# Performance work log

Hardware: AMD Instinct MI355X
Metric: run time of the kernel (lower is better)

The kernel has to match this reference:

```python
import jax, jax.numpy as jnp
import numpy as np
from jax import lax

FI, FO, K, EPS = 512, 256, 3, 1e-06


def _fir_kernel(gain):
    f = jnp.array([1.0, 3.0, 3.0, 1.0], dtype=jnp.float32)
    f = f[None, :] * f[:, None]
    f = f / f.sum() * gain  # (4,4), symmetric so conv-vs-correlation flip is a no-op
    return f


def setup_inputs() -> dict:
    key = jax.random.key(0)
    k1, k2 = jax.random.split(key)
    x = jax.random.normal(k1, (8, FI, 64, 64), dtype=jnp.float32)
    w = jax.random.normal(k2, (1, FO, FI, K, K), dtype=jnp.float32)
    return {"x": x, "w": w}


def reference(x, w):
    w_scale = (FI * K * K) ** (-0.5)
    wm = w[0] * w_scale  # (fo, fi, k, k); per-sample scale is constant across batch
    demod = lax.rsqrt(jnp.sum(wm * wm, axis=(1, 2, 3)) + EPS)  # (fo,)
    wm = wm * demod[:, None, None, None]
    # torch conv_transpose2d(stride=2, padding=0) with weight (fi, fo, k, k) where
    # weight[i, o] = wm[o, i]  ==  dilated conv with kernel flip(wm) OIHW, pad k-1=2.
    kern = wm[:, :, ::-1, ::-1]
    y = lax.conv_general_dilated(
        x, kern, window_strides=(1, 1), padding=[(2, 2), (2, 2)],
        lhs_dilation=(2, 2), dimension_numbers=("NCHW", "OIHW", "NCHW"))
    # upFirDn2D with scale=2, conv_k=3: p=0 -> pad (1,1) both dims, filter gain 4
    f = _fir_kernel(4.0)
    C = y.shape[1]
    fk = jnp.broadcast_to(f[None, None], (C, 1, 4, 4))
    y = lax.conv_general_dilated(
        y, fk, window_strides=(1, 1), padding=[(1, 1), (1, 1)],
        feature_group_count=C, dimension_numbers=("NCHW", "OIHW", "NCHW"))
    return y  # (8, 256, 128, 128)
```

## Files before the change

kernel.cpp:

```cpp
#include <hip/hip_runtime.h>

typedef unsigned short u16;
typedef unsigned int u32;
typedef __attribute__((ext_vector_type(8))) short bf16x8;
typedef __attribute__((ext_vector_type(4))) float f32x4;

#define XP_BYTES 35684352
#define YB_BYTES 68714544
#define HY_OFF   (XP_BYTES + YB_BYTES)
#define WS_NEED  ((size_t)HY_OFF + 2359296)
#define CS 16776

__device__ inline u16 f2bf(float f) {
  union { float f; unsigned u; } v; v.f = f;
  unsigned r = v.u + 0x7fffu + ((v.u >> 16) & 1u);
  return (u16)(r >> 16);
}

__device__ inline void gl_lds16(const u16* g, u16* l) {
  __builtin_amdgcn_global_load_lds(
      (const __attribute__((address_space(1))) unsigned int*)g,
      (__attribute__((address_space(3))) unsigned int*)l, 16, 0, 0);
}

__global__ void xprep(const float* __restrict__ x, u16* __restrict__ xp) {
  __shared__ float tile[64 * 65];
  int bid = blockIdx.x;
  int cc = bid & 7, h = (bid >> 3) & 63, n = bid >> 9;
  int c0 = cc * 64;
  int t = threadIdx.x;
  const float* xb = x + ((size_t)(n * 512 + c0) * 64 + h) * 64;
  for (int r = 0; r < 16; ++r) {
    int flat = r * 256 + t;
    int ci = flat >> 6, w = flat & 63;
    tile[w * 65 + ci] = xb[(size_t)ci * 4096 + w];
  }
  __syncthreads();
  u16* xpb = xp + ((size_t)(n * 66 + h + 1) * 66 + 1) * 512 + c0;
  for (int r = 0; r < 8; ++r) {
    int flat = r * 256 + t;
    int pr = flat & 31;
    int w = flat >> 5;
    int ci = pr * 2;
    float v0 = tile[w * 65 + ci], v1 = tile[w * 65 + ci + 1];
    unsigned pk = (unsigned)f2bf(v0) | ((unsigned)f2bf(v1) << 16);
    *(unsigned*)(xpb + (size_t)w * 512 + ci) = pk;
  }
  u16* rowbase = xp + ((size_t)(n * 66 + h + 1) * 66) * 512 + c0;
  if (t < 32) *(u32*)(rowbase + 2 * t) = 0u;
  else if (t < 64) *(u32*)(rowbase + (size_t)65 * 512 + 2 * (t - 32)) = 0u;
  if (h == 0) {
    u16* r0 = xp + ((size_t)(n * 66) * 66) * 512 + c0;
    for (int j = t; j < 2112; j += 256) {
      int col = j >> 5, wi = j & 31;
      *(u32*)(r0 + (size_t)col * 512 + 2 * wi) = 0u;
    }
  }
  if (h == 63) {
    u16* r65 = xp + ((size_t)(n * 66 + 65) * 66) * 512 + c0;
    for (int j = t; j < 2112; j += 256) {
      int col = j >> 5, wi = j & 31;
      *(u32*)(r65 + (size_t)col * 512 + 2 * wi) = 0u;
    }
  }
}

__global__ void wprep9(const float* __restrict__ w, u16* __restrict__ Hy) {
  __shared__ float wl[4608];
  __shared__ float red[256];
  int o = blockIdx.x, t = threadIdx.x;
  const float* wo = w + (size_t)o * 4608;
  float s = 0.f;
  for (int j = t; j < 4608; j += 256) { float v = wo[j]; wl[j] = v; s += v * v; }
  red[t] = s;
  __syncthreads();
  for (int st = 128; st; st >>= 1) { if (t < st) red[t] += red[t + st]; __syncthreads(); }
  float demod = rsqrtf(red[0] * (1.0f / 4608.0f) + 1e-6f);
  float scale = demod * 0.014731391274719739f;
  const int DY[9] = {0, 2, 0, 2, 0, 2, 1, 1, 1};
  const int DX[9] = {0, 0, 2, 2, 1, 1, 0, 2, 1};
  for (int i = t; i < 512; i += 256) {
#pragma unroll
    for (int pl = 0; pl < 9; ++pl) {
      float g = wl[i * 9 + DY[pl] * 3 + DX[pl]] * scale;
      Hy[(size_t)pl * 131072 + (size_t)o * 512 + i] = f2bf(g);
    }
  }
}

#define BARR() __builtin_amdgcn_s_barrier()
#define WAITL() do { asm volatile("s_waitcnt lgkmcnt(0)" ::: "memory"); __builtin_amdgcn_sched_barrier(0); } while (0)
#define WAITV1() do { asm volatile("s_waitcnt vmcnt(1)" ::: "memory"); __builtin_amdgcn_sched_barrier(0); } while (0)
#define WAITV0() do { asm volatile("s_waitcnt vmcnt(0)" ::: "memory"); __builtin_amdgcn_sched_barrier(0); } while (0)

__device__ __forceinline__ void rdA4(const u16* sbA, int la, int grp, int hi,
                                     bf16x8 af[4]) {
#pragma unroll
  for (int ti = 0; ti < 4; ++ti) {
    int p = ti * 16 + la;
    int slot = (hi * 4 + grp) ^ (p & 7);
    af[ti] = *(const bf16x8*)(sbA + p * 64 + slot * 8);
  }
}

__device__ __forceinline__ bf16x8 rdB1(const u16* sb, int r, int grp) {
  int p = r & 63, hi = r >> 6;
  int slot = (hi * 4 + grp) ^ (p & 7);
  return *(const bf16x8*)(sb + 8192 + p * 64 + slot * 8);
}

template <int MI, int NI>
__device__ __forceinline__ void qmfma4(const bf16x8 af[4], bf16x8 bf,
                                       f32x4 acc[8][2]) {
#pragma unroll
  for (int ti = 0; ti < 4; ++ti)
    acc[MI * 4 + ti][NI] = __builtin_amdgcn_mfma_f32_16x16x32_bf16(
        af[ti], bf, acc[MI * 4 + ti][NI], 0, 0, 0);
}

__device__ __forceinline__ void stA1(const u16* __restrict__ xp, u16* d,
                                     int tile, int NK, u32 a,
                                     u32 adj1, u32 adj2, u32 adj3) {
  if (tile < NK) {
    int tap = tile >> 4;
    u32 ko = (u32)((tile & 15) << 5);
    u32 adj = tap == 0 ? 0u : (tap == 1 ? adj1 : (tap == 2 ? adj2 : adj3));
    gl_lds16(xp + (a - adj + ko), d);
  }
}

__device__ __forceinline__ void stB1(const u16* __restrict__ hb, u16* d,
                                     int tile, int NK, u32 b) {
  if (tile < NK) {
    int tap = tile >> 4;
    u32 ko = (u32)((tile & 15) << 5);
    gl_lds16(hb + (size_t)tap * 131072 + (b + ko), d);
  }
}

__global__ __launch_bounds__(512, 4) void conv_y(const u16* __restrict__ xp,
                                                 const u16* __restrict__ Hy,
                                                 u16* __restrict__ yb) {
  __shared__ __align__(16) u16 su[24576];

  int bid = blockIdx.x;
  int t = threadIdx.x;
  int wid = t >> 6, lane = t & 63;

  int img = bid & 7;
  int kk = bid >> 3;
  int mt, oh, Wp, CNT, NTAP, PB, PO, STLIM;
  u32 adj1 = 0, adj2 = 0, adj3 = 0;
  if (kk < 34)       { int k2 = kk;       mt = k2 >> 1; oh = k2 & 1; Wp = 66; CNT = 4290; NTAP = 4; PB = 0; PO = 0;     STLIM = 4296;
                       adj1 = 33792u; adj2 = 512u; adj3 = 34304u; }
  else if (kk < 68)  { int k2 = kk - 34;  mt = k2 >> 1; oh = k2 & 1; Wp = 64; CNT = 4160; NTAP = 2; PB = 4; PO = 4296;  STLIM = 4160;
                       adj1 = 33792u; }
  else if (kk < 102) { int k2 = kk - 68;  mt = k2 >> 1; oh = k2 & 1; Wp = 66; CNT = 4224; NTAP = 2; PB = 6; PO = 8456;  STLIM = 4224;
                       adj1 = 512u; }
  else               { int k2 = kk - 102; mt = k2 >> 1; oh = k2 & 1; Wp = 64; CNT = 4096; NTAP = 1; PB = 8; PO = 12680; STLIM = 4096; }

  int m0 = mt * 256;
  int o0 = oh * 128;
  int NK = NTAP * 16;
  int NITER = NTAP * 8;
  const u16* hb = Hy + (size_t)PB * 131072;

  int wm = wid >> 2, wn = wid & 3;
  int la = lane & 15, grp = lane >> 4;

  int sp = t >> 3;
  int se = (t & 7) ^ (sp & 7);
  int shi = se >> 2, sc = se & 3;
  int sloc = shi * 64 + sp;

  u32 gA0, gA1, gB;
  {
    int m = m0 + sloc;
    if (m > CNT - 1) m = CNT - 1;
    u32 a = (u32)m / (u32)Wp;
    u32 b = (u32)m - a * (u32)Wp;
    gA0 = (u32)(((img * 66 + a + 1) * 66 + (b + 1)) * 512 + sc * 8);
    m = m0 + 128 + sloc;
    if (m > CNT - 1) m = CNT - 1;
    a = (u32)m / (u32)Wp;
    b = (u32)m - a * (u32)Wp;
    gA1 = (u32)(((img * 66 + a + 1) * 66 + (b + 1)) * 512 + sc * 8);
    gB = (u32)((o0 + sloc) * 512 + sc * 8);
  }
  int ws = wid * 512;

  f32x4 acc[8][2];
#pragma unroll
  for (int i = 0; i < 8; ++i)
#pragma unroll
    for (int j = 0; j < 2; ++j) acc[i][j] = (f32x4){0.f, 0.f, 0.f, 0.f};

  stB1(hb, su + 8192 + ws, 0, NK, gB);
  stA1(xp, su + 0 + ws, 0, NK, gA0, adj1, adj2, adj3);
  stA1(xp, su + 4096 + ws, 0, NK, gA1, adj1, adj2, adj3);
  stB1(hb, su + 20480 + ws, 1, NK, gB);
  WAITV1();
  BARR();

  bf16x8 af[4], bf0, bf1;

#pragma unroll 1
  for (int it = 0; it < NITER; ++it) {
    int t0 = 2 * it;
    bool more = (it + 1 < NITER);

    rdA4(su + wm * 4096, la, grp, 0, af);
    bf0 = rdB1(su, wn * 32 + la, grp);
    stA1(xp, su + 12288 + ws, t0 + 1, NK, gA0, adj1, adj2, adj3);
    BARR(); WAITL();
    __builtin_amdgcn_s_setprio(1); qmfma4<0, 0>(af, bf0, acc); __builtin_amdgcn_s_setprio(0);
    BARR();
    bf1 = rdB1(su, wn * 32 + 16 + la, grp);
    stA1(xp, su + 16384 + ws, t0 + 1, NK, gA1, adj1, adj2, adj3);
    BARR(); WAITL();
    __builtin_amdgcn_s_setprio(1); qmfma4<0, 1>(af, bf1, acc); __builtin_amdgcn_s_setprio(0);
    BARR();
    rdA4(su + wm * 4096, la, grp, 1, af);
    stB1(hb, su + 8192 + ws, t0 + 2, NK, gB);
    BARR(); WAITL();
    __builtin_amdgcn_s_setprio(1);
    qmfma4<1, 1>(af, bf1, acc); qmfma4<1, 0>(af, bf0, acc);
    __builtin_amdgcn_s_setprio(0);
    if (more) { WAITV1(); } else { WAITV0(); }
    BARR();
    rdA4(su + 12288 + wm * 4096, la, grp, 0, af);
    bf0 = rdB1(su + 12288, wn * 32 + la, grp);
    stA1(xp, su + 0 + ws, t0 + 2, NK, gA0, adj1, adj2, adj3);
    BARR(); WAITL();
    __builtin_amdgcn_s_setprio(1); qmfma4<0, 0>(af, bf0, acc); __builtin_amdgcn_s_setprio(0);
    BARR();
    bf1 = rdB1(su + 12288, wn * 32 + 16 + la, grp);
    stA1(xp, su + 4096 + ws, t0 + 2, NK, gA1, adj1, adj2, adj3);
    BARR(); WAITL();
    __builtin_amdgcn_s_setprio(1); qmfma4<0, 1>(af, bf1, acc); __builtin_amdgcn_s_setprio(0);
    BARR();
    rdA4(su + 12288 + wm * 4096, la, grp, 1, af);
    stB1(hb, su + 20480 + ws, t0 + 3, NK, gB);
    BARR(); WAITL();
    __builtin_amdgcn_s_setprio(1);
    qmfma4<1, 1>(af, bf1, acc); qmfma4<1, 0>(af, bf0, acc);
    __builtin_amdgcn_s_setprio(0);
    if (more) { WAITV1(); }
    BARR();
  }

  WAITV0();
  __syncthreads();
  u16* ybp = yb + 8;
#pragma unroll 1
  for (int r = 0; r < 2; ++r) {
    if ((wn >> 1) == r) {
      int base_orl = (wn & 1) * 32;
#pragma unroll
      for (int nj = 0; nj < 2; ++nj) {
        int orl = base_orl + nj * 16 + la;
        int x7 = orl & 7;
#pragma unroll
        for (int mi8 = 0; mi8 < 8; ++mi8)
#pragma unroll
          for (int jp = 0; jp < 2; ++jp) {
            int ml = wm * 128 + mi8 * 16 + grp * 4 + jp * 2;
            u32 pk = (u32)f2bf(acc[mi8][nj][jp * 2]) |
                     ((u32)f2bf(acc[mi8][nj][jp * 2 + 1]) << 16);
            *(u32*)(su + orl * 256 + (((ml >> 3) ^ x7) * 8) + (ml & 7)) = pk;
          }
      }
    }
    __syncthreads();
    {
      int ol = t >> 3, s2 = t & 7;
      int og = o0 + r * 64 + ol;
      size_t gb = (size_t)(img * 256 + og) * CS + PO + m0;
      int x7 = ol & 7;
#pragma unroll
      for (int i = 0; i < 4; ++i) {
        int cidx = s2 * 4 + i;
        int m = cidx * 8;
        if (m0 + m < STLIM)
          *(bf16x8*)(ybp + gb + m) = *(const bf16x8*)(su + ol * 256 + ((cidx ^ x7) * 8));
      }
    }
    if (r == 0) __syncthreads();
  }
}

__global__ void fir2(const u16* __restrict__ yb, float* __restrict__ z) {
  int flat = blockIdx.x * 256 + threadIdx.x;
  int qh = flat & 15, phb = (flat >> 4) & 31, o = (flat >> 9) & 255, n = flat >> 17;
  const u16* cb = yb + 8 + (size_t)(n * 256 + o) * CS;
  int a0 = 2 * phb - 1;
  int b0 = 4 * qh - 1;

  float out[4][8];
#pragma unroll
  for (int i = 0; i < 4; ++i)
#pragma unroll
    for (int j = 0; j < 8; ++j) out[i][j] = 0.f;

  const int PO_[4] = {0, 4296, 8456, 12680};
  const int WP_[4] = {66, 64, 66, 64};
  const int HA_[4] = {65, 65, 64, 64};
  const int WB_[4] = {65, 64, 65, 64};

#pragma unroll
  for (int ph = 0; ph < 4; ++ph) {
    int rp = ph >> 1, rq = ph & 1;
    const u16* pb = cb + PO_[ph];
    float hcol[4][8];
#pragma unroll
    for (int la = 0; la < 4; ++la) {
      if (rp == 0 && la == 0) continue;
      int ag = a0 + la;
      bool rv = (ag >= 0) && (ag < HA_[ph]);
      const u16* rb = pb + (ag * WP_[ph] + b0 - 1);
      u32 ls[4];
      ls[0] = *(const u32*)(rb);
      ls[1] = *(const u32*)(rb + 2);
      ls[2] = *(const u32*)(rb + 4);
      ls[3] = *(const u32*)(rb + 6);
      float v[6];
#pragma unroll
      for (int lb = 0; lb < 6; ++lb) {
        int jj = lb + 1;
        u32 w16 = (jj & 1) ? (ls[jj >> 1] >> 16) : (ls[jj >> 1] & 0xffffu);
        float fv = __uint_as_float(w16 << 16);
        int bg = b0 + lb;
        bool ok = rv && (bg >= 0) && (bg < WB_[ph]);
        v[lb] = ok ? fv : 0.f;
      }
#pragma unroll
      for (int e = 0; e < 4; ++e) {
        if (rq == 0) {
          hcol[la][2 * e]     = 3.f * v[e + 1] + v[e + 2];
          hcol[la][2 * e + 1] = v[e + 1] + 3.f * v[e + 2];
        } else {
          hcol[la][2 * e]     = v[e] + 3.f * v[e + 1];
          hcol[la][2 * e + 1] = 3.f * v[e + 1] + v[e + 2];
        }
      }
    }
#pragma unroll
    for (int jq = 0; jq < 8; ++jq) {
      if (rp == 0) {
        out[0][jq] += 3.f * hcol[1][jq] + hcol[2][jq];
        out[1][jq] += hcol[1][jq] + 3.f * hcol[2][jq];
        out[2][jq] += 3.f * hcol[2][jq] + hcol[3][jq];
        out[3][jq] += hcol[2][jq] + 3.f * hcol[3][jq];
      } else {
        out[0][jq] += hcol[0][jq] + 3.f * hcol[1][jq];
        out[1][jq] += 3.f * hcol[1][jq] + hcol[2][jq];
        out[2][jq] += hcol[1][jq] + 3.f * hcol[2][jq];
        out[3][jq] += 3.f * hcol[2][jq] + hcol[3][jq];
      }
    }
  }

  float* zb = z + ((size_t)(n * 256 + o) * 128 + phb * 4) * 128 + qh * 8;
#pragma unroll
  for (int ip = 0; ip < 4; ++ip) {
    f32x4 v0, v1;
#pragma unroll
    for (int j = 0; j < 4; ++j) { v0[j] = out[ip][j] * 0.0625f; v1[j] = out[ip][j + 4] * 0.0625f; }
    *(f32x4*)(zb + (size_t)ip * 128) = v0;
    *(f32x4*)(zb + (size_t)ip * 128 + 4) = v1;
  }
}

__global__ void wprep36(const float* __restrict__ w, u16* __restrict__ Hm) {
  __shared__ float wl[4608];
  __shared__ float red[256];
  int o = blockIdx.x, t = threadIdx.x;
  const float* wo = w + (size_t)o * 4608;
  float s = 0.f;
  for (int j = t; j < 4608; j += 256) { float v = wo[j]; wl[j] = v; s += v * v; }
  red[t] = s;
  __syncthreads();
  for (int st = 128; st; st >>= 1) { if (t < st) red[t] += red[t + st]; __syncthreads(); }
  float demod = rsqrtf(red[0] * (1.0f / 4608.0f) + 1e-6f);
  float scale = demod * 0.014731391274719739f;
  const float F1[4] = {1.f, 3.f, 3.f, 1.f};
  for (int i = t; i < 512; i += 256) {
    float wm[9];
    for (int k = 0; k < 9; ++k) wm[k] = wl[i * 9 + k] * scale;
    for (int rp = 0; rp < 2; ++rp)
      for (int rq = 0; rq < 2; ++rq)
        for (int u = 0; u < 3; ++u)
          for (int v = 0; v < 3; ++v) {
            int s_ = 2 - 2 * u + rp, t_ = 2 - 2 * v + rq;
            float g = 0.f;
            for (int dy = 0; dy < 3; ++dy) {
              int a = dy + 1 - s_;
              if (a < 0 || a > 3) continue;
              for (int dx = 0; dx < 3; ++dx) {
                int b = dx + 1 - t_;
                if (b < 0 || b > 3) continue;
                g += wm[dy * 3 + dx] * (F1[a] * F1[b]);
              }
            }
            g *= 0.0625f;
            Hm[(size_t)((rp * 2 + rq) * 9 + u * 3 + v) * 131072 + (size_t)o * 512 + i] = f2bf(g);
          }
  }
}

__global__ __launch_bounds__(256) void conv_main(const u16* __restrict__ xp,
                                                 const u16* __restrict__ Hm,
                                                 float* __restrict__ z) {
  __shared__ __align__(16) float smemf[8448];
  u16* su = (u16*)smemf;
  int bid = blockIdx.x;
  int sub = bid & 7;
  int rp = sub >> 2;
  int o0 = (sub & 3) * 64;
  int mtile = bid >> 3;
  int n_img = mtile >> 5;
  int hp0 = (mtile & 31) * 2;
  int t = threadIdx.x;
  int wave = t >> 6, lane = t & 63;
  int wm0 = (wave & 1) * 64;
  int wn0 = (wave >> 1) * 32;
  int la = lane & 15;
  int ks = (lane >> 4) * 8;
  int rsel = t >> 2;
  int koff = (t & 3) * 8;
  f32x4 acc[2][4][2];
#pragma unroll
  for (int a = 0; a < 2; ++a)
#pragma unroll
    for (int b = 0; b < 4; ++b)
#pragma unroll
      for (int c = 0; c < 2; ++c)
        acc[a][b][c] = (f32x4){0.f, 0.f, 0.f, 0.f};
#pragma unroll 1
  for (int tap = 0; tap < 9; ++tap) {
    int du = tap / 3, dv = tap - du * 3;
    const u16* gA0 = xp + ((size_t)(n_img * 66 + hp0 + du) * 66 + dv) * 512;
    const u16* gB0 = Hm + (size_t)(rp * 18 + tap) * 131072 + (size_t)(o0 + rsel) * 512 + koff;
    const u16* gAr0 = gA0 + (size_t)rsel * 512 + koff;
    const u16* gAr1 = gA0 + (size_t)(66 + rsel) * 512 + koff;
#pragma unroll 1
    for (int kc = 0; kc < 16; ++kc) {
      int c0 = kc * 32;
      __syncthreads();
      gl_lds16(gAr0 + c0, su + wave * 512);
      gl_lds16(gAr1 + c0, su + 2048 + wave * 512);
      gl_lds16(gB0 + c0,              su + 4096 + wave * 512);
      gl_lds16(gB0 + 9 * 131072 + c0, su + 6144 + wave * 512);
      __syncthreads();
      bf16x8 af[4];
#pragma unroll
      for (int ti = 0; ti < 4; ++ti)
        af[ti] = *(const bf16x8*)(su + (wm0 + ti * 16 + la) * 32 + ks);
      bf16x8 bfr[2][2];
#pragma unroll
      for (int rqq = 0; rqq < 2; ++rqq)
#pragma unroll
        for (int tj = 0; tj < 2; ++tj)
          bfr[rqq][tj] = *(const bf16x8*)(su + 4096 + rqq * 2048 + (wn0 + tj * 16 + la) * 32 + ks);
#pragma unroll
      for (int rqq = 0; rqq < 2; ++rqq)
#pragma unroll
        for (int ti = 0; ti < 4; ++ti)
#pragma unroll
          for (int tj = 0; tj < 2; ++tj)
            acc[rqq][ti][tj] = __builtin_amdgcn_mfma_f32_16x16x32_bf16(
                af[ti], bfr[rqq][tj], acc[rqq][ti][tj], 0, 0, 0);
    }
  }
  __syncthreads();
  float* lws = smemf + wave * 2112;
  int p = 2 * (hp0 + (wave & 1)) + rp;
#pragma unroll
  for (int tj = 0; tj < 2; ++tj) {
#pragma unroll
    for (int rqq = 0; rqq < 2; ++rqq)
#pragma unroll
      for (int ti = 0; ti < 4; ++ti) {
        int wqb = ti * 16 + (lane >> 4) * 4;
        f32x4 v = acc[rqq][ti][tj];
#pragma unroll
        for (int r = 0; r < 4; ++r)
          lws[la * 132 + 2 * (wqb + r) + rqq] = v[r];
      }
    __syncthreads();
    int obase = o0 + wn0 + tj * 16;
#pragma unroll
    for (int c = 0; c < 8; ++c) {
      int idx = c * 64 + lane;
      int ol = idx >> 5, q4 = (idx & 31) * 4;
      f32x4 vv = *(const f32x4*)(lws + ol * 132 + q4);
      *(f32x4*)(z + (((size_t)n_img * 256 + obase + ol) * 128 + p) * 128 + q4) = vv;
    }
    __syncthreads();
  }
}

extern "C" void kernel_launch(void* const* d_in, const int* in_sizes, int n_in,
                              void* d_out, int out_size, void* d_ws, size_t ws_size,
                              hipStream_t stream) {
  const float* x = (const float*)d_in[0];
  const float* w = (const float*)d_in[1];
  float* z = (float*)d_out;
  u16* xp = (u16*)d_ws;

  if (ws_size >= WS_NEED) {
    u16* yb = (u16*)((char*)d_ws + XP_BYTES);
    u16* hy = (u16*)((char*)d_ws + HY_OFF);
    xprep<<<4096, 256, 0, stream>>>(x, xp);
    wprep9<<<256, 256, 0, stream>>>(w, hy);
    conv_y<<<1072, 512, 0, stream>>>(xp, hy, yb);
    fir2<<<4096, 256, 0, stream>>>(yb, z);
  } else {
    u16* Hm = (u16*)((char*)d_ws + XP_BYTES);
    hipMemsetAsync(xp, 0, XP_BYTES, stream);
    xprep<<<4096, 256, 0, stream>>>(x, xp);
    wprep36<<<256, 256, 0, stream>>>(w, Hm);
    conv_main<<<2048, 256, 0, stream>>>(xp, Hm, z);
  }
}
```

Before: 322.1 us.

## Switch padded input and weight planes to channel-chunked 32-wide layout

Changes the bf16 padded input from NHWC with 512 contiguous channels to 16 planes of 32-channel chunks per image, and the per-tap weights to matching 32-channel chunk planes. Global-to-LDS loads then fetch from a compact plane per K-tile, which changes how many rows and pages each tile's loads span and may improve cache and TLB locality. The fallback path keeps the old layout through a copied xprep_flat kernel. Stores in xprep become more scattered, and correctness depends on the new offsets matching the LDS tile layout.

```diff
diff --git a/kernel.cpp b/kernel.cpp
--- a/kernel.cpp
+++ b/kernel.cpp
@@ -36,7 +36,6 @@
     tile[w * 65 + ci] = xb[(size_t)ci * 4096 + w];
   }
   __syncthreads();
-  u16* xpb = xp + ((size_t)(n * 66 + h + 1) * 66 + 1) * 512 + c0;
   for (int r = 0; r < 8; ++r) {
     int flat = r * 256 + t;
     int pr = flat & 31;
@@ -44,23 +43,31 @@
     int ci = pr * 2;
     float v0 = tile[w * 65 + ci], v1 = tile[w * 65 + ci + 1];
     unsigned pk = (unsigned)f2bf(v0) | ((unsigned)f2bf(v1) << 16);
-    *(unsigned*)(xpb + (size_t)w * 512 + ci) = pk;
-  }
-  u16* rowbase = xp + ((size_t)(n * 66 + h + 1) * 66) * 512 + c0;
-  if (t < 32) *(u32*)(rowbase + 2 * t) = 0u;
-  else if (t < 64) *(u32*)(rowbase + (size_t)65 * 512 + 2 * (t - 32)) = 0u;
-  if (h == 0) {
-    u16* r0 = xp + ((size_t)(n * 66) * 66) * 512 + c0;
+    int kcabs = cc * 2 + (ci >> 5);
+    int chl = ci & 31;
+    u16* dst = xp + (size_t)(n * 16 + kcabs) * 139392 +
+               (size_t)((h + 1) * 66 + (w + 1)) * 32 + chl;
+    *(unsigned*)dst = pk;
+  }
+  if (t < 64) {
+    int seg = t >> 4;
+    int colsel = (seg >> 1) ? 65 : 0;
+    int pl = cc * 2 + (seg & 1);
+    int ui = t & 15;
+    u16* dst = xp + (size_t)(n * 16 + pl) * 139392 +
+               (size_t)((h + 1) * 66 + colsel) * 32 + ui * 2;
+    *(u32*)dst = 0u;
+  }
+  if (h == 0 || h == 63) {
+    int rowbase = (h == 0) ? 0 : 65 * 66;
     for (int j = t; j < 2112; j += 256) {
-      int col = j >> 5, wi = j & 31;
-      *(u32*)(r0 + (size_t)col * 512 + 2 * wi) = 0u;
-    }
-  }
-  if (h == 63) {
-    u16* r65 = xp + ((size_t)(n * 66 + 65) * 66) * 512 + c0;
-    for (int j = t; j < 2112; j += 256) {
-      int col = j >> 5, wi = j & 31;
-      *(u32*)(r65 + (size_t)col * 512 + 2 * wi) = 0u;
+      int seg = j >> 4;
+      int ui = j & 15;
+      int pl = cc * 2 + (seg & 1);
+      int pos = seg >> 1;
+      u16* dst = xp + (size_t)(n * 16 + pl) * 139392 +
+                 (size_t)(rowbase + pos) * 32 + ui * 2;
+      *(u32*)dst = 0u;
     }
   }
 }
@@ -80,10 +87,11 @@
   const int DY[9] = {0, 2, 0, 2, 0, 2, 1, 1, 1};
   const int DX[9] = {0, 0, 2, 2, 1, 1, 0, 2, 1};
   for (int i = t; i < 512; i += 256) {
+    int kc = i >> 5, il = i & 31;
 #pragma unroll
     for (int pl = 0; pl < 9; ++pl) {
       float g = wl[i * 9 + DY[pl] * 3 + DX[pl]] * scale;
-      Hy[(size_t)pl * 131072 + (size_t)o * 512 + i] = f2bf(g);
+      Hy[(size_t)(pl * 16 + kc) * 8192 + (size_t)o * 32 + il] = f2bf(g);
     }
   }
 }
@@ -123,9 +131,9 @@
                                      u32 adj1, u32 adj2, u32 adj3) {
   if (tile < NK) {
     int tap = tile >> 4;
-    u32 ko = (u32)((tile & 15) << 5);
+    u32 ko = (u32)((tile & 15) * 139392);
     u32 adj = tap == 0 ? 0u : (tap == 1 ? adj1 : (tap == 2 ? adj2 : adj3));
-    gl_lds16(xp + (a - adj + ko), d);
+    gl_lds16(xp + (a + ko - adj), d);
   }
 }
 
@@ -133,8 +141,8 @@
                                      int tile, int NK, u32 b) {
   if (tile < NK) {
     int tap = tile >> 4;
-    u32 ko = (u32)((tile & 15) << 5);
-    gl_lds16(hb + (size_t)tap * 131072 + (b + ko), d);
+    u32 ko = (u32)(tap * 131072 + (tile & 15) * 8192);
+    gl_lds16(hb + (b + ko), d);
   }
 }
 
@@ -152,11 +160,11 @@
   int mt, oh, Wp, CNT, NTAP, PB, PO, STLIM;
   u32 adj1 = 0, adj2 = 0, adj3 = 0;
   if (kk < 34)       { int k2 = kk;       mt = k2 >> 1; oh = k2 & 1; Wp = 66; CNT = 4290; NTAP = 4; PB = 0; PO = 0;     STLIM = 4296;
-                       adj1 = 33792u; adj2 = 512u; adj3 = 34304u; }
+                       adj1 = 2112u; adj2 = 32u; adj3 = 2144u; }
   else if (kk < 68)  { int k2 = kk - 34;  mt = k2 >> 1; oh = k2 & 1; Wp = 64; CNT = 4160; NTAP = 2; PB = 4; PO = 4296;  STLIM = 4160;
-                       adj1 = 33792u; }
+                       adj1 = 2112u; }
   else if (kk < 102) { int k2 = kk - 68;  mt = k2 >> 1; oh = k2 & 1; Wp = 66; CNT = 4224; NTAP = 2; PB = 6; PO = 8456;  STLIM = 4224;
-                       adj1 = 512u; }
+                       adj1 = 32u; }
   else               { int k2 = kk - 102; mt = k2 >> 1; oh = k2 & 1; Wp = 64; CNT = 4096; NTAP = 1; PB = 8; PO = 12680; STLIM = 4096; }
 
   int m0 = mt * 256;
@@ -175,17 +183,18 @@
 
   u32 gA0, gA1, gB;
   {
+    u32 ib = (u32)img * 2230272u;
     int m = m0 + sloc;
     if (m > CNT - 1) m = CNT - 1;
     u32 a = (u32)m / (u32)Wp;
     u32 b = (u32)m - a * (u32)Wp;
-    gA0 = (u32)(((img * 66 + a + 1) * 66 + (b + 1)) * 512 + sc * 8);
+    gA0 = ib + ((a + 1) * 66 + (b + 1)) * 32 + sc * 8;
     m = m0 + 128 + sloc;
     if (m > CNT - 1) m = CNT - 1;
     a = (u32)m / (u32)Wp;
     b = (u32)m - a * (u32)Wp;
-    gA1 = (u32)(((img * 66 + a + 1) * 66 + (b + 1)) * 512 + sc * 8);
-    gB = (u32)((o0 + sloc) * 512 + sc * 8);
+    gA1 = ib + ((a + 1) * 66 + (b + 1)) * 32 + sc * 8;
+    gB = (u32)((o0 + sloc) * 32 + sc * 8);
   }
   int ws = wid * 512;
 
@@ -371,6 +380,48 @@
   }
 }
 
+__global__ void xprep_flat(const float* __restrict__ x, u16* __restrict__ xp) {
+  __shared__ float tile[64 * 65];
+  int bid = blockIdx.x;
+  int cc = bid & 7, h = (bid >> 3) & 63, n = bid >> 9;
+  int c0 = cc * 64;
+  int t = threadIdx.x;
+  const float* xb = x + ((size_t)(n * 512 + c0) * 64 + h) * 64;
+  for (int r = 0; r < 16; ++r) {
+    int flat = r * 256 + t;
+    int ci = flat >> 6, w = flat & 63;
+    tile[w * 65 + ci] = xb[(size_t)ci * 4096 + w];
+  }
+  __syncthreads();
+  u16* xpb = xp + ((size_t)(n * 66 + h + 1) * 66 + 1) * 512 + c0;
+  for (int r = 0; r < 8; ++r) {
+    int flat = r * 256 + t;
+    int pr = flat & 31;
+    int w = flat >> 5;
+    int ci = pr * 2;
+    float v0 = tile[w * 65 + ci], v1 = tile[w * 65 + ci + 1];
+    unsigned pk = (unsigned)f2bf(v0) | ((unsigned)f2bf(v1) << 16);
+    *(unsigned*)(xpb + (size_t)w * 512 + ci) = pk;
+  }
+  u16* rowbase = xp + ((size_t)(n * 66 + h + 1) * 66) * 512 + c0;
+  if (t < 32) *(u32*)(rowbase + 2 * t) = 0u;
+  else if (t < 64) *(u32*)(rowbase + (size_t)65 * 512 + 2 * (t - 32)) = 0u;
+  if (h == 0) {
+    u16* r0 = xp + ((size_t)(n * 66) * 66) * 512 + c0;
+    for (int j = t; j < 2112; j += 256) {
+      int col = j >> 5, wi = j & 31;
+      *(u32*)(r0 + (size_t)col * 512 + 2 * wi) = 0u;
+    }
+  }
+  if (h == 63) {
+    u16* r65 = xp + ((size_t)(n * 66 + 65) * 66) * 512 + c0;
+    for (int j = t; j < 2112; j += 256) {
+      int col = j >> 5, wi = j & 31;
+      *(u32*)(r65 + (size_t)col * 512 + 2 * wi) = 0u;
+    }
+  }
+}
+
 __global__ void wprep36(const float* __restrict__ w, u16* __restrict__ Hm) {
   __shared__ float wl[4608];
   __shared__ float red[256];
@@ -518,7 +569,7 @@
   } else {
     u16* Hm = (u16*)((char*)d_ws + XP_BYTES);
     hipMemsetAsync(xp, 0, XP_BYTES, stream);
-    xprep<<<4096, 256, 0, stream>>>(x, xp);
+    xprep_flat<<<4096, 256, 0, stream>>>(x, xp);
     wprep36<<<256, 256, 0, stream>>>(w, Hm);
     conv_main<<<2048, 256, 0, stream>>>(xp, Hm, z);
   }
```

Result: faster. 311.6 us (-3.3%).
